# Kernel tuning notes

Hardware: AMD Instinct MI355X
Metric: run time of the kernel (lower is better)

## Reference

```python
import jax, jax.numpy as jnp
import numpy as np

HEADS = 8
EPS = 1e-4

def pixel_norm(x):
    # faithful to source: mean over dim=1 (token axis for [B,T,C] tensors)
    return x / jnp.sqrt(jnp.mean(x * x, axis=1, keepdims=True) + EPS)

def setup_inputs() -> dict:
    key = jax.random.key(0)
    ks = jax.random.split(key, 6)
    B, T, C = 4, 2048, 512
    s = 1.0 / np.sqrt(C)
    return {
        "hidden_states": jax.random.normal(ks[0], (B, T, C), jnp.float32),
        "Wq": jax.random.normal(ks[1], (C, C), jnp.float32) * s,
        "Wk": jax.random.normal(ks[2], (C, C), jnp.float32) * s,
        "Wv": jax.random.normal(ks[3], (C, C), jnp.float32) * s,
        "Wo": jax.random.normal(ks[4], (C, C), jnp.float32) * s,
        "bo": jnp.zeros((C,), jnp.float32),
    }

def reference(hidden_states, Wq, Wk, Wv, Wo, bo):
    B, T, C = hidden_states.shape
    H = HEADS
    d = C // H
    scale = 1.0 / np.sqrt(d)  # attn.scale = head_dim**-0.5
    residual = hidden_states

    q = pixel_norm(hidden_states @ Wq)  # [B,T,C]
    k = pixel_norm(hidden_states @ Wk)
    v = pixel_norm(hidden_states @ Wv)

    # head_to_batch_dim: [B,T,C] -> [B,H,T,d]
    def split_heads(x):
        return x.reshape(B, T, H, d).transpose(0, 2, 1, 3)
    q, k, v = split_heads(q), split_heads(k), split_heads(v)

    scores = jnp.einsum("bhqd,bhkd->bhqk", q, k) * scale
    probs = jax.nn.softmax(scores, axis=-1)
    out = jnp.einsum("bhqk,bhkd->bhqd", probs, v)  # [B,H,T,d]

    # batch_to_head_dim: [B,H,T,d] -> [B,T,C]
    out = out.transpose(0, 2, 1, 3).reshape(B, T, C)
    out = out @ Wo + bo  # to_out[0]; to_out[1] is dropout (identity in eval)
    out = out + residual  # residual_connection
    return out  # rescale_output_factor = 1.0
```

## Files before the change

### kernel.cpp

```cpp
#include <hip/hip_runtime.h>

#define Tt 2048
#define Cc 512
#define Bb 4
#define BC (Bb * Cc)

typedef __attribute__((ext_vector_type(4))) float f32x4;
typedef __attribute__((ext_vector_type(8))) _Float16 f16x8;
typedef __attribute__((ext_vector_type(4))) _Float16 f16x4;
typedef __attribute__((ext_vector_type(2))) _Float16 f16x2;

__global__ __launch_bounds__(256) void wsetup(
    const float* __restrict__ Wq, const float* __restrict__ Wk,
    const float* __restrict__ Wv, const float* __restrict__ Wo,
    _Float16* __restrict__ Wt)
{
    const int z = blockIdx.y;
    const float* W = (z == 0) ? Wq : (z == 1) ? Wk : (z == 2) ? Wv : Wo;
    const int k0 = (blockIdx.x >> 3) * 64, n0 = (blockIdx.x & 7) * 64;
    const int tid = threadIdx.x;
    __shared__ float tile[64][65];

#pragma unroll
    for (int i = 0; i < 4; ++i) {
        const int idx = i * 256 + tid;
        const int kr = idx >> 4, c4 = idx & 15;
        float4 v = *(const float4*)&W[(size_t)(k0 + kr) * Cc + n0 + c4 * 4];
        tile[kr][c4 * 4 + 0] = v.x; tile[kr][c4 * 4 + 1] = v.y;
        tile[kr][c4 * 4 + 2] = v.z; tile[kr][c4 * 4 + 3] = v.w;
    }
    __syncthreads();
#pragma unroll
    for (int i = 0; i < 4; ++i) {
        const int idx = i * 256 + tid;
        const int nr = idx >> 4, k4 = idx & 15;
        f16x4 o;
        o[0] = (_Float16)tile[k4 * 4 + 0][nr];
        o[1] = (_Float16)tile[k4 * 4 + 1][nr];
        o[2] = (_Float16)tile[k4 * 4 + 2][nr];
        o[3] = (_Float16)tile[k4 * 4 + 3][nr];
        *(f16x4*)&Wt[((size_t)(z * 512 + n0 + nr)) * Cc + k0 + k4 * 4] = o;
    }
}

__global__ __launch_bounds__(256, 3) void qkv_mfma(
    const float* __restrict__ HS, const _Float16* __restrict__ Wt,
    _Float16* __restrict__ Qf, _Float16* __restrict__ Kf,
    _Float16* __restrict__ Vf, float* __restrict__ colsum)
{
    const int mt = blockIdx.x;
    const int nt = blockIdx.y;
    const int z  = blockIdx.z;
    _Float16* Out = (z == 0) ? Qf : (z == 1) ? Kf : Vf;

    const int tid = threadIdx.x;
    const int wave = tid >> 6, lane = tid & 63;
    const int quad = lane >> 4, lm = lane & 15;
    const int wm = (wave & 1) * 64, wn = (wave >> 1) * 64;

    __shared__ _Float16 sA[128 * 40];
    __shared__ _Float16 sB[128 * 40];

    f32x4 acc[4][4];
#pragma unroll
    for (int mf = 0; mf < 4; ++mf)
#pragma unroll
        for (int nf = 0; nf < 4; ++nf) acc[mf][nf] = (f32x4){0.f, 0.f, 0.f, 0.f};

    const int r2 = tid >> 1, kc = (tid & 1) * 16;
    const float* ga = HS + (size_t)(mt * 128 + r2) * Cc + kc;
    const _Float16* gb = Wt + ((size_t)(z * 512 + nt * 128 + r2)) * Cc + kc;

    for (int k0 = 0; k0 < Cc; k0 += 32) {
        __syncthreads();
        {
            float4 a0 = *(const float4*)&ga[k0];
            float4 a1 = *(const float4*)&ga[k0 + 4];
            float4 a2 = *(const float4*)&ga[k0 + 8];
            float4 a3 = *(const float4*)&ga[k0 + 12];
            f16x8 h0, h1;
            h0[0] = (_Float16)a0.x; h0[1] = (_Float16)a0.y;
            h0[2] = (_Float16)a0.z; h0[3] = (_Float16)a0.w;
            h0[4] = (_Float16)a1.x; h0[5] = (_Float16)a1.y;
            h0[6] = (_Float16)a1.z; h0[7] = (_Float16)a1.w;
            h1[0] = (_Float16)a2.x; h1[1] = (_Float16)a2.y;
            h1[2] = (_Float16)a2.z; h1[3] = (_Float16)a2.w;
            h1[4] = (_Float16)a3.x; h1[5] = (_Float16)a3.y;
            h1[6] = (_Float16)a3.z; h1[7] = (_Float16)a3.w;
            *(f16x8*)&sA[r2 * 40 + kc]     = h0;
            *(f16x8*)&sA[r2 * 40 + kc + 8] = h1;
            *(f16x8*)&sB[r2 * 40 + kc]     = *(const f16x8*)&gb[k0];
            *(f16x8*)&sB[r2 * 40 + kc + 8] = *(const f16x8*)&gb[k0 + 8];
        }
        __syncthreads();

        f16x8 ah[4], bh[4];
#pragma unroll
        for (int mf = 0; mf < 4; ++mf)
            ah[mf] = *(const f16x8*)&sA[(wm + mf * 16 + lm) * 40 + quad * 8];
#pragma unroll
        for (int nf = 0; nf < 4; ++nf)
            bh[nf] = *(const f16x8*)&sB[(wn + nf * 16 + lm) * 40 + quad * 8];
#pragma unroll
        for (int mf = 0; mf < 4; ++mf)
#pragma unroll
            for (int nf = 0; nf < 4; ++nf)
                acc[mf][nf] = __builtin_amdgcn_mfma_f32_16x16x32_f16(ah[mf], bh[nf], acc[mf][nf], 0, 0, 0);
    }

    const int bidx = mt >> 4;
#pragma unroll
    for (int nf = 0; nf < 4; ++nf) {
        float cs = 0.f;
#pragma unroll
        for (int mf = 0; mf < 4; ++mf)
#pragma unroll
            for (int r = 0; r < 4; ++r) {
                const float v = acc[mf][nf][r];
                const size_t idx =
                    (size_t)(mt * 128 + wm + mf * 16 + quad * 4 + r) * Cc +
                    nt * 128 + wn + nf * 16 + lm;
                Out[idx] = (_Float16)v;
                cs += v * v;
            }
        cs += __shfl_xor(cs, 16, 64);
        cs += __shfl_xor(cs, 32, 64);
        if (lane < 16)
            atomicAdd(&colsum[(size_t)z * BC + bidx * Cc + nt * 128 + wn + nf * 16 + lane], cs);
    }
}

__global__ void inv_norm_kernel(const float* __restrict__ colsum,
                                float* __restrict__ inv)
{
    const int i = blockIdx.x * blockDim.x + threadIdx.x;
    if (i < 3 * BC) inv[i] = rsqrtf(colsum[i] * (1.0f / Tt) + 1e-4f);
}

__global__ __launch_bounds__(256) void norm_vt(
    const _Float16* __restrict__ V, _Float16* __restrict__ VT)
{
    const int blk = blockIdx.x;
    const int b = blk >> 8, ct = (blk >> 5) & 7, tt = blk & 31;
    const int t0 = tt * 64, c0 = ct * 64;
    const int tid = threadIdx.x;

    __shared__ _Float16 tile[64 * 72];

#pragma unroll
    for (int i = 0; i < 2; ++i) {
        const int idx = i * 256 + tid;
        const int tr = idx >> 3, c8 = (idx & 7) * 8;
        *(f16x8*)&tile[tr * 72 + c8] =
            *(const f16x8*)&V[(size_t)(b * Tt + t0 + tr) * Cc + c0 + c8];
    }
    __syncthreads();
#pragma unroll
    for (int i = 0; i < 2; ++i) {
        const int idx = i * 256 + tid;
        const int cr = idx >> 3, t8 = (idx & 7) * 8;
        f16x8 o;
#pragma unroll
        for (int j = 0; j < 8; ++j) o[j] = tile[(t8 + j) * 72 + cr];
        *(f16x8*)&VT[(size_t)(b * Cc + c0 + cr) * Tt + t0 + t8] = o;
    }
}

#define LSTR 72

__global__ __launch_bounds__(256, 2) void attn_mfma(
    const _Float16* __restrict__ Qf, const _Float16* __restrict__ Kf,
    const _Float16* __restrict__ VT, const float* __restrict__ inv,
    _Float16* __restrict__ AO)
{
    const int bid = blockIdx.x;
    const int qt = bid >> 5;
    const int bh = bid & 31;
    const int b = bh >> 3, h = bh & 7;
    const int tid = threadIdx.x;
    const int wave = tid >> 6, lane = tid & 63;
    const int quad = lane >> 4, lm = lane & 15;

    __shared__ _Float16 sK[2][64 * LSTR];
    __shared__ _Float16 sVT[2][64 * LSTR];
    __shared__ _Float16 sP[2][4][32 * LSTR];

    f16x8 qb[2][2];
    {
        const float* iqp = inv + b * Cc + h * 64;
        const float* ikp = inv + BC + b * Cc + h * 64;
#pragma unroll
        for (int qf = 0; qf < 2; ++qf) {
            const int row = qt * 128 + wave * 32 + qf * 16 + lm;
#pragma unroll
            for (int ks = 0; ks < 2; ++ks) {
                const int d0 = ks * 32 + quad * 8;
                f16x8 qv = *(const f16x8*)&Qf[(size_t)(b * Tt + row) * Cc + h * 64 + d0];
#pragma unroll
                for (int j = 0; j < 8; ++j) {
                    const float f = (float)qv[j] * iqp[d0 + j] * ikp[d0 + j] * 0.18033688011f;
                    qb[qf][ks][j] = (_Float16)f;
                }
            }
        }
    }

    f32x4 o[4][2];
#pragma unroll
    for (int cf = 0; cf < 4; ++cf)
#pragma unroll
        for (int qf = 0; qf < 2; ++qf) o[cf][qf] = (f32x4){0.f, 0.f, 0.f, 0.f};
    f32x4 ol[2];
#pragma unroll
    for (int qf = 0; qf < 2; ++qf) ol[qf] = (f32x4){0.f, 0.f, 0.f, 0.f};
    f16x8 ones;
#pragma unroll
    for (int j = 0; j < 8; ++j) ones[j] = (_Float16)1.0f;

    const int sr0 = tid >> 3, sc0 = (tid & 7) * 8;
    const int sr1 = sr0 + 32;
    const _Float16* gK = Kf + (size_t)b * Tt * Cc + h * 64;
    const _Float16* gV = VT + ((size_t)b * Cc + h * 64) * Tt;

    f16x8 rk0, rk1, rv0, rv1;
    {
        rk0 = *(const f16x8*)&gK[(size_t)sr0 * Cc + sc0];
        rk1 = *(const f16x8*)&gK[(size_t)sr1 * Cc + sc0];
        rv0 = *(const f16x8*)&gV[(size_t)sr0 * Tt + sc0];
        rv1 = *(const f16x8*)&gV[(size_t)sr1 * Tt + sc0];
    }

    for (int kt = 0; kt < 32; ++kt) {
        const int cur = kt & 1, prv = cur ^ 1;
        _Float16* sKc = sK[cur];
        _Float16* sVc = sVT[cur];
        _Float16* myPc = &sP[cur][wave][0];
        _Float16* myPp = &sP[prv][wave][0];

        __syncthreads();
        *(f16x8*)&sKc[sr0 * LSTR + sc0] = rk0;
        *(f16x8*)&sKc[sr1 * LSTR + sc0] = rk1;
        *(f16x8*)&sVc[sr0 * LSTR + sc0] = rv0;
        *(f16x8*)&sVc[sr1 * LSTR + sc0] = rv1;
        __syncthreads();

        if (kt < 31) {
            const int t0 = (kt + 1) * 64;
            rk0 = *(const f16x8*)&gK[(size_t)(t0 + sr0) * Cc + sc0];
            rk1 = *(const f16x8*)&gK[(size_t)(t0 + sr1) * Cc + sc0];
            rv0 = *(const f16x8*)&gV[(size_t)sr0 * Tt + t0 + sc0];
            rv1 = *(const f16x8*)&gV[(size_t)sr1 * Tt + t0 + sc0];
        }

        f32x4 st[4][2];
#pragma unroll
        for (int kf = 0; kf < 4; ++kf)
#pragma unroll
            for (int qf = 0; qf < 2; ++qf) st[kf][qf] = (f32x4){0.f, 0.f, 0.f, 0.f};
#pragma unroll
        for (int ks = 0; ks < 2; ++ks) {
            f16x8 ka[4];
#pragma unroll
            for (int kf = 0; kf < 4; ++kf)
                ka[kf] = *(const f16x8*)&sKc[(kf * 16 + lm) * LSTR + ks * 32 + quad * 8];
#pragma unroll
            for (int kf = 0; kf < 4; ++kf)
#pragma unroll
                for (int qf = 0; qf < 2; ++qf)
                    st[kf][qf] = __builtin_amdgcn_mfma_f32_16x16x32_f16(ka[kf], qb[qf][ks], st[kf][qf], 0, 0, 0);
        }

        if (kt > 0) {
            _Float16* sVp = sVT[prv];
#pragma unroll
            for (int ks = 0; ks < 2; ++ks) {
                f16x8 pb[2];
#pragma unroll
                for (int qf = 0; qf < 2; ++qf)
                    pb[qf] = *(const f16x8*)&myPp[(qf * 16 + lm) * LSTR + ks * 32 + quad * 8];
                f16x8 va[4];
#pragma unroll
                for (int cf = 0; cf < 4; ++cf)
                    va[cf] = *(const f16x8*)&sVp[(cf * 16 + lm) * LSTR + ks * 32 + quad * 8];
#pragma unroll
                for (int cf = 0; cf < 4; ++cf)
#pragma unroll
                    for (int qf = 0; qf < 2; ++qf)
                        o[cf][qf] = __builtin_amdgcn_mfma_f32_16x16x32_f16(va[cf], pb[qf], o[cf][qf], 0, 0, 0);
#pragma unroll
                for (int qf = 0; qf < 2; ++qf)
                    ol[qf] = __builtin_amdgcn_mfma_f32_16x16x32_f16(ones, pb[qf], ol[qf], 0, 0, 0);
            }
        }

#pragma unroll
        for (int kf = 0; kf < 4; ++kf)
#pragma unroll
            for (int qf = 0; qf < 2; ++qf) {
                const float p0 = __builtin_amdgcn_exp2f(st[kf][qf][0]);
                const float p1 = __builtin_amdgcn_exp2f(st[kf][qf][1]);
                const float p2 = __builtin_amdgcn_exp2f(st[kf][qf][2]);
                const float p3 = __builtin_amdgcn_exp2f(st[kf][qf][3]);
                const f16x2 lo = __builtin_bit_cast(f16x2, __builtin_amdgcn_cvt_pkrtz(p0, p1));
                const f16x2 hi = __builtin_bit_cast(f16x2, __builtin_amdgcn_cvt_pkrtz(p2, p3));
                f16x4 pk;
                pk[0] = lo[0]; pk[1] = lo[1]; pk[2] = hi[0]; pk[3] = hi[1];
                *(f16x4*)&myPc[(qf * 16 + lm) * LSTR + kf * 16 + quad * 4] = pk;
            }
    }

    {
        _Float16* myPp = &sP[1][wave][0];
        _Float16* sVp = sVT[1];
#pragma unroll
        for (int ks = 0; ks < 2; ++ks) {
            f16x8 pb[2];
#pragma unroll
            for (int qf = 0; qf < 2; ++qf)
                pb[qf] = *(const f16x8*)&myPp[(qf * 16 + lm) * LSTR + ks * 32 + quad * 8];
            f16x8 va[4];
#pragma unroll
            for (int cf = 0; cf < 4; ++cf)
                va[cf] = *(const f16x8*)&sVp[(cf * 16 + lm) * LSTR + ks * 32 + quad * 8];
#pragma unroll
            for (int cf = 0; cf < 4; ++cf)
#pragma unroll
                for (int qf = 0; qf < 2; ++qf)
                    o[cf][qf] = __builtin_amdgcn_mfma_f32_16x16x32_f16(va[cf], pb[qf], o[cf][qf], 0, 0, 0);
#pragma unroll
            for (int qf = 0; qf < 2; ++qf)
                ol[qf] = __builtin_amdgcn_mfma_f32_16x16x32_f16(ones, pb[qf], ol[qf], 0, 0, 0);
        }
    }

    float il[2];
#pragma unroll
    for (int qf = 0; qf < 2; ++qf) il[qf] = 1.0f / ol[qf][0];
    const float* ivp = inv + 2 * BC + b * Cc + h * 64;
    float iv[4][4];
#pragma unroll
    for (int cf = 0; cf < 4; ++cf) {
        float4 t = *(const float4*)&ivp[cf * 16 + quad * 4];
        iv[cf][0] = t.x; iv[cf][1] = t.y; iv[cf][2] = t.z; iv[cf][3] = t.w;
    }
#pragma unroll
    for (int qf = 0; qf < 2; ++qf) {
        const size_t row = (size_t)(b * Tt + qt * 128 + wave * 32 + qf * 16 + lm);
#pragma unroll
        for (int cf = 0; cf < 4; ++cf) {
            f16x4 pk;
#pragma unroll
            for (int r = 0; r < 4; ++r)
                pk[r] = (_Float16)(o[cf][qf][r] * il[qf] * iv[cf][r]);
            *(f16x4*)&AO[row * Cc + h * 64 + cf * 16 + quad * 4] = pk;
        }
    }
}

__global__ __launch_bounds__(256, 2) void out_mfma(
    const _Float16* __restrict__ AO, const _Float16* __restrict__ Wt,
    const float* __restrict__ bo, const float* __restrict__ HS,
    float* __restrict__ Outp)
{
    const int mt = blockIdx.x;
    const int nt = blockIdx.y;
    const int tid = threadIdx.x;
    const int wave = tid >> 6, lane = tid & 63;
    const int quad = lane >> 4, lm = lane & 15;
    const int wm = (wave & 1) * 32, wn = (wave >> 1) * 64;

    __shared__ _Float16 sA[64 * 40];
    __shared__ _Float16 sB[128 * 40];

    f32x4 acc[2][4];
#pragma unroll
    for (int mf = 0; mf < 2; ++mf)
#pragma unroll
        for (int nf = 0; nf < 4; ++nf) acc[mf][nf] = (f32x4){0.f, 0.f, 0.f, 0.f};

    const int ra = tid >> 2, ka = (tid & 3) * 8;
    const int rb = tid >> 1, kb = (tid & 1) * 16;
    const _Float16* gah = AO + (size_t)(mt * 64 + ra) * Cc + ka;
    const _Float16* gbh = Wt + ((size_t)(3 * 512 + nt * 128 + rb)) * Cc + kb;

    for (int k0 = 0; k0 < Cc; k0 += 32) {
        __syncthreads();
        {
            *(f16x8*)&sA[ra * 40 + ka] = *(const f16x8*)&gah[k0];
            *(f16x8*)&sB[rb * 40 + kb]     = *(const f16x8*)&gbh[k0];
            *(f16x8*)&sB[rb * 40 + kb + 8] = *(const f16x8*)&gbh[k0 + 8];
        }
        __syncthreads();

        f16x8 ah[2], bh[4];
#pragma unroll
        for (int mf = 0; mf < 2; ++mf)
            ah[mf] = *(const f16x8*)&sA[(wm + mf * 16 + lm) * 40 + quad * 8];
#pragma unroll
        for (int nf = 0; nf < 4; ++nf)
            bh[nf] = *(const f16x8*)&sB[(wn + nf * 16 + lm) * 40 + quad * 8];
#pragma unroll
        for (int mf = 0; mf < 2; ++mf)
#pragma unroll
            for (int nf = 0; nf < 4; ++nf)
                acc[mf][nf] = __builtin_amdgcn_mfma_f32_16x16x32_f16(ah[mf], bh[nf], acc[mf][nf], 0, 0, 0);
    }

#pragma unroll
    for (int mf = 0; mf < 2; ++mf)
#pragma unroll
        for (int r = 0; r < 4; ++r) {
            const size_t m = (size_t)(mt * 64 + wm + mf * 16 + quad * 4 + r);
#pragma unroll
            for (int nf = 0; nf < 4; ++nf) {
                const int col = nt * 128 + wn + nf * 16 + lm;
                Outp[m * Cc + col] = acc[mf][nf][r] + bo[col] + HS[m * Cc + col];
            }
        }
}

extern "C" void kernel_launch(void* const* d_in, const int* in_sizes, int n_in,
                              void* d_out, int out_size, void* d_ws,
                              size_t ws_size, hipStream_t stream)
{
    const float* HS = (const float*)d_in[0];
    const float* Wq = (const float*)d_in[1];
    const float* Wk = (const float*)d_in[2];
    const float* Wv = (const float*)d_in[3];
    const float* Wo = (const float*)d_in[4];
    const float* bo = (const float*)d_in[5];
    float* out = (float*)d_out;

    const size_t SZ = (size_t)Bb * Tt * Cc;
    _Float16* Qf  = (_Float16*)d_ws;
    _Float16* Kf  = Qf + SZ;
    _Float16* Vf  = Kf + SZ;
    _Float16* VTh = Vf + SZ;
    _Float16* AO  = VTh + SZ;
    _Float16* Wt  = AO + SZ;
    float* colsum = (float*)(Wt + 4 * Cc * Cc);
    float* inv    = colsum + 3 * BC;

    (void)hipMemsetAsync(colsum, 0, 3 * BC * sizeof(float), stream);

    wsetup<<<dim3(64, 4), 256, 0, stream>>>(Wq, Wk, Wv, Wo, Wt);

    qkv_mfma<<<dim3(64, 4, 3), 256, 0, stream>>>(HS, Wt, Qf, Kf, Vf, colsum);

    inv_norm_kernel<<<(3 * BC + 255) / 256, 256, 0, stream>>>(colsum, inv);

    norm_vt<<<1024, 256, 0, stream>>>(Vf, VTh);

    attn_mfma<<<dim3(512), 256, 0, stream>>>(Qf, Kf, VTh, inv, AO);

    out_mfma<<<dim3(128, 4), 256, 0, stream>>>(AO, Wt, bo, HS, out);
}
```

Measured before the change: 181.6 us.

## Keep attention probabilities in registers, pre-convert hidden states to fp16, permute V^T layout

The attention kernel no longer round-trips softmax probabilities through shared memory. The V^T transpose writes keys in a permuted order so that the MFMA score-accumulator layout can be packed directly into the B operand of the PV MFMA. Removing the shared P buffer frees LDS, so the occupancy hint goes from 2 to 3 blocks per SM. A separate kernel converts hidden states to fp16 once into the VT scratch buffer, so the QKV GEMM's 12 blocks that share each row tile no longer each redo the fp32 load and conversion. The cost is an extra kernel launch, and the higher occupancy target may add register pressure.

After: 167.0 us. 8.1% less time.

```diff
diff --git a/kernel.cpp b/kernel.cpp
--- a/kernel.cpp
+++ b/kernel.cpp
@@ -43,8 +43,22 @@
     }
 }
 
+__global__ __launch_bounds__(256) void hs_half(
+    const float* __restrict__ HS, _Float16* __restrict__ HSh)
+{
+    const size_t i = ((size_t)blockIdx.x * 256 + threadIdx.x) * 8;
+    float4 a = *(const float4*)&HS[i];
+    float4 b = *(const float4*)&HS[i + 4];
+    f16x8 o;
+    o[0] = (_Float16)a.x; o[1] = (_Float16)a.y;
+    o[2] = (_Float16)a.z; o[3] = (_Float16)a.w;
+    o[4] = (_Float16)b.x; o[5] = (_Float16)b.y;
+    o[6] = (_Float16)b.z; o[7] = (_Float16)b.w;
+    *(f16x8*)&HSh[i] = o;
+}
+
 __global__ __launch_bounds__(256, 3) void qkv_mfma(
-    const float* __restrict__ HS, const _Float16* __restrict__ Wt,
+    const _Float16* __restrict__ HSh, const _Float16* __restrict__ Wt,
     _Float16* __restrict__ Qf, _Float16* __restrict__ Kf,
     _Float16* __restrict__ Vf, float* __restrict__ colsum)
 {
@@ -68,27 +82,14 @@
         for (int nf = 0; nf < 4; ++nf) acc[mf][nf] = (f32x4){0.f, 0.f, 0.f, 0.f};
 
     const int r2 = tid >> 1, kc = (tid & 1) * 16;
-    const float* ga = HS + (size_t)(mt * 128 + r2) * Cc + kc;
+    const _Float16* ga = HSh + (size_t)(mt * 128 + r2) * Cc + kc;
     const _Float16* gb = Wt + ((size_t)(z * 512 + nt * 128 + r2)) * Cc + kc;
 
     for (int k0 = 0; k0 < Cc; k0 += 32) {
         __syncthreads();
         {
-            float4 a0 = *(const float4*)&ga[k0];
-            float4 a1 = *(const float4*)&ga[k0 + 4];
-            float4 a2 = *(const float4*)&ga[k0 + 8];
-            float4 a3 = *(const float4*)&ga[k0 + 12];
-            f16x8 h0, h1;
-            h0[0] = (_Float16)a0.x; h0[1] = (_Float16)a0.y;
-            h0[2] = (_Float16)a0.z; h0[3] = (_Float16)a0.w;
-            h0[4] = (_Float16)a1.x; h0[5] = (_Float16)a1.y;
-            h0[6] = (_Float16)a1.z; h0[7] = (_Float16)a1.w;
-            h1[0] = (_Float16)a2.x; h1[1] = (_Float16)a2.y;
-            h1[2] = (_Float16)a2.z; h1[3] = (_Float16)a2.w;
-            h1[4] = (_Float16)a3.x; h1[5] = (_Float16)a3.y;
-            h1[6] = (_Float16)a3.z; h1[7] = (_Float16)a3.w;
-            *(f16x8*)&sA[r2 * 40 + kc]     = h0;
-            *(f16x8*)&sA[r2 * 40 + kc + 8] = h1;
+            *(f16x8*)&sA[r2 * 40 + kc]     = *(const f16x8*)&ga[k0];
+            *(f16x8*)&sA[r2 * 40 + kc + 8] = *(const f16x8*)&ga[k0 + 8];
             *(f16x8*)&sB[r2 * 40 + kc]     = *(const f16x8*)&gb[k0];
             *(f16x8*)&sB[r2 * 40 + kc + 8] = *(const f16x8*)&gb[k0 + 8];
         }
@@ -158,17 +159,22 @@
 #pragma unroll
     for (int i = 0; i < 2; ++i) {
         const int idx = i * 256 + tid;
-        const int cr = idx >> 3, t8 = (idx & 7) * 8;
-        f16x8 o;
-#pragma unroll
-        for (int j = 0; j < 8; ++j) o[j] = tile[(t8 + j) * 72 + cr];
-        *(f16x8*)&VT[(size_t)(b * Cc + c0 + cr) * Tt + t0 + t8] = o;
+        const int cr = idx >> 3, u = idx & 7;
+        const int C0 = ((u >> 2) & 1) * 32 + (u & 1) * 16 + ((u >> 1) & 1) * 4;
+        f16x4 oa, ob;
+#pragma unroll
+        for (int j = 0; j < 4; ++j) oa[j] = tile[(u * 8 + j) * 72 + cr];
+#pragma unroll
+        for (int j = 0; j < 4; ++j) ob[j] = tile[(u * 8 + 4 + j) * 72 + cr];
+        _Float16* dst = &VT[(size_t)(b * Cc + c0 + cr) * Tt + t0];
+        *(f16x4*)&dst[C0]     = oa;
+        *(f16x4*)&dst[C0 + 8] = ob;
     }
 }
 
 #define LSTR 72
 
-__global__ __launch_bounds__(256, 2) void attn_mfma(
+__global__ __launch_bounds__(256, 3) void attn_mfma(
     const _Float16* __restrict__ Qf, const _Float16* __restrict__ Kf,
     const _Float16* __restrict__ VT, const float* __restrict__ inv,
     _Float16* __restrict__ AO)
@@ -183,7 +189,6 @@
 
     __shared__ _Float16 sK[2][64 * LSTR];
     __shared__ _Float16 sVT[2][64 * LSTR];
-    __shared__ _Float16 sP[2][4][32 * LSTR];
 
     f16x8 qb[2][2];
     {
@@ -216,6 +221,14 @@
     f16x8 ones;
 #pragma unroll
     for (int j = 0; j < 8; ++j) ones[j] = (_Float16)1.0f;
+
+    f16x8 pb[2][2];
+#pragma unroll
+    for (int qf = 0; qf < 2; ++qf)
+#pragma unroll
+        for (int ks = 0; ks < 2; ++ks)
+#pragma unroll
+            for (int j = 0; j < 8; ++j) pb[qf][ks][j] = (_Float16)0.0f;
 
     const int sr0 = tid >> 3, sc0 = (tid & 7) * 8;
     const int sr1 = sr0 + 32;
@@ -234,8 +247,6 @@
         const int cur = kt & 1, prv = cur ^ 1;
         _Float16* sKc = sK[cur];
         _Float16* sVc = sVT[cur];
-        _Float16* myPc = &sP[cur][wave][0];
-        _Float16* myPp = &sP[prv][wave][0];
 
         __syncthreads();
         *(f16x8*)&sKc[sr0 * LSTR + sc0] = rk0;
@@ -274,10 +285,6 @@
             _Float16* sVp = sVT[prv];
 #pragma unroll
             for (int ks = 0; ks < 2; ++ks) {
-                f16x8 pb[2];
-#pragma unroll
-                for (int qf = 0; qf < 2; ++qf)
-                    pb[qf] = *(const f16x8*)&myPp[(qf * 16 + lm) * LSTR + ks * 32 + quad * 8];
                 f16x8 va[4];
 #pragma unroll
                 for (int cf = 0; cf < 4; ++cf)
@@ -286,38 +293,38 @@
                 for (int cf = 0; cf < 4; ++cf)
 #pragma unroll
                     for (int qf = 0; qf < 2; ++qf)
-                        o[cf][qf] = __builtin_amdgcn_mfma_f32_16x16x32_f16(va[cf], pb[qf], o[cf][qf], 0, 0, 0);
+                        o[cf][qf] = __builtin_amdgcn_mfma_f32_16x16x32_f16(va[cf], pb[qf][ks], o[cf][qf], 0, 0, 0);
 #pragma unroll
                 for (int qf = 0; qf < 2; ++qf)
-                    ol[qf] = __builtin_amdgcn_mfma_f32_16x16x32_f16(ones, pb[qf], ol[qf], 0, 0, 0);
+                    ol[qf] = __builtin_amdgcn_mfma_f32_16x16x32_f16(ones, pb[qf][ks], ol[qf], 0, 0, 0);
             }
         }
 
 #pragma unroll
-        for (int kf = 0; kf < 4; ++kf)
+        for (int ks = 0; ks < 2; ++ks)
 #pragma unroll
             for (int qf = 0; qf < 2; ++qf) {
-                const float p0 = __builtin_amdgcn_exp2f(st[kf][qf][0]);
-                const float p1 = __builtin_amdgcn_exp2f(st[kf][qf][1]);
-                const float p2 = __builtin_amdgcn_exp2f(st[kf][qf][2]);
-                const float p3 = __builtin_amdgcn_exp2f(st[kf][qf][3]);
-                const f16x2 lo = __builtin_bit_cast(f16x2, __builtin_amdgcn_cvt_pkrtz(p0, p1));
-                const f16x2 hi = __builtin_bit_cast(f16x2, __builtin_amdgcn_cvt_pkrtz(p2, p3));
-                f16x4 pk;
-                pk[0] = lo[0]; pk[1] = lo[1]; pk[2] = hi[0]; pk[3] = hi[1];
-                *(f16x4*)&myPc[(qf * 16 + lm) * LSTR + kf * 16 + quad * 4] = pk;
+                const f32x4 a = st[2 * ks][qf];
+                const f32x4 c = st[2 * ks + 1][qf];
+                const f16x2 l0 = __builtin_bit_cast(f16x2, __builtin_amdgcn_cvt_pkrtz(
+                    __builtin_amdgcn_exp2f(a[0]), __builtin_amdgcn_exp2f(a[1])));
+                const f16x2 l1 = __builtin_bit_cast(f16x2, __builtin_amdgcn_cvt_pkrtz(
+                    __builtin_amdgcn_exp2f(a[2]), __builtin_amdgcn_exp2f(a[3])));
+                const f16x2 h0 = __builtin_bit_cast(f16x2, __builtin_amdgcn_cvt_pkrtz(
+                    __builtin_amdgcn_exp2f(c[0]), __builtin_amdgcn_exp2f(c[1])));
+                const f16x2 h1 = __builtin_bit_cast(f16x2, __builtin_amdgcn_cvt_pkrtz(
+                    __builtin_amdgcn_exp2f(c[2]), __builtin_amdgcn_exp2f(c[3])));
+                f16x8 p;
+                p[0] = l0[0]; p[1] = l0[1]; p[2] = l1[0]; p[3] = l1[1];
+                p[4] = h0[0]; p[5] = h0[1]; p[6] = h1[0]; p[7] = h1[1];
+                pb[qf][ks] = p;
             }
     }
 
     {
-        _Float16* myPp = &sP[1][wave][0];
         _Float16* sVp = sVT[1];
 #pragma unroll
         for (int ks = 0; ks < 2; ++ks) {
-            f16x8 pb[2];
-#pragma unroll
-            for (int qf = 0; qf < 2; ++qf)
-                pb[qf] = *(const f16x8*)&myPp[(qf * 16 + lm) * LSTR + ks * 32 + quad * 8];
             f16x8 va[4];
 #pragma unroll
             for (int cf = 0; cf < 4; ++cf)
@@ -326,10 +333,10 @@
             for (int cf = 0; cf < 4; ++cf)
 #pragma unroll
                 for (int qf = 0; qf < 2; ++qf)
-                    o[cf][qf] = __builtin_amdgcn_mfma_f32_16x16x32_f16(va[cf], pb[qf], o[cf][qf], 0, 0, 0);
+                    o[cf][qf] = __builtin_amdgcn_mfma_f32_16x16x32_f16(va[cf], pb[qf][ks], o[cf][qf], 0, 0, 0);
 #pragma unroll
             for (int qf = 0; qf < 2; ++qf)
-                ol[qf] = __builtin_amdgcn_mfma_f32_16x16x32_f16(ones, pb[qf], ol[qf], 0, 0, 0);
+                ol[qf] = __builtin_amdgcn_mfma_f32_16x16x32_f16(ones, pb[qf][ks], ol[qf], 0, 0, 0);
         }
     }
 
@@ -441,11 +448,15 @@
     float* colsum = (float*)(Wt + 4 * Cc * Cc);
     float* inv    = colsum + 3 * BC;
 
+    _Float16* HSh = VTh;
+
     (void)hipMemsetAsync(colsum, 0, 3 * BC * sizeof(float), stream);
 
     wsetup<<<dim3(64, 4), 256, 0, stream>>>(Wq, Wk, Wv, Wo, Wt);
 
-    qkv_mfma<<<dim3(64, 4, 3), 256, 0, stream>>>(HS, Wt, Qf, Kf, Vf, colsum);
+    hs_half<<<2048, 256, 0, stream>>>(HS, HSh);
+
+    qkv_mfma<<<dim3(64, 4, 3), 256, 0, stream>>>(HSh, Wt, Qf, Kf, Vf, colsum);
 
     inv_norm_kernel<<<(3 * BC + 255) / 256, 256, 0, stream>>>(colsum, inv);
 
```
